# Performance work log

Hardware: AMD Instinct MI355X
Metric: run time of the kernel (lower is better)

Reference implementation:

```python
import jax, jax.numpy as jnp
import numpy as np

H_IMG, W_IMG = 224, 224  # image_size default in forward


def setup_inputs() -> dict:
    key = jax.random.key(0)
    k0, k1, k2 = jax.random.split(key, 3)
    B, C, M, N = 4, 256, 1024, 16384
    xyz_feats = jax.random.normal(k0, (B, C, M), jnp.float32)
    # projections land inside the image for a realistic bin distribution
    points = jax.random.uniform(k1, (B, N, 3), jnp.float32).at[..., 2].add(0.5)
    centers = jax.random.uniform(k2, (B, M, 3), jnp.float32).at[..., 2].add(0.5)
    fx = fy = 0.5 * W_IMG  # plausible intrinsics already scaled to 224x224
    K = jnp.array([[fx, 0.0, W_IMG / 2.0],
                   [0.0, fy, H_IMG / 2.0],
                   [0.0, 0.0, 1.0]], jnp.float32)
    return {"xyz_feats": xyz_feats, "points": points, "centers": centers,
            "K": K, "kernel_size": 4}


def reference(xyz_feats, points, centers, K, kernel_size):
    B, C, M = xyz_feats.shape
    N = points.shape[1]
    H, W = H_IMG, W_IMG

    # --- interpolating_points: PointNet++ 3-NN inverse-distance interp ---
    # squared pairwise distances [B, N, M]
    d2 = (jnp.sum(points * points, -1)[:, :, None]
          + jnp.sum(centers * centers, -1)[:, None, :]
          - 2.0 * jnp.einsum('bnd,bmd->bnm', points, centers))
    neg_d, idx = jax.lax.top_k(-d2, 3)            # 3 nearest centers, [B,N,3]
    w = 1.0 / (-neg_d + 1e-8)                     # inverse-distance weights
    w = w / jnp.sum(w, -1, keepdims=True)
    b3 = jnp.arange(B)[:, None, None]
    gathered = xyz_feats[b3, :, idx]              # [B, N, 3, C]
    interp = jnp.einsum('bnkc,bnk->bnc', gathered, w)  # [B, N, C]

    # --- project_to_image ---
    uvz = jnp.einsum('ij,bnj->bni', K, points)    # [B, N, 3]
    uv = uvz[..., :2] / jnp.maximum(uvz[..., 2:], 1e-8)
    u = jnp.clip(jnp.floor(uv[..., 0]), 0, W - 1).astype(jnp.int32)
    v = jnp.clip(jnp.floor(uv[..., 1]), 0, H - 1).astype(jnp.int32)
    idx_flat = u + v * W                          # [B, N]

    # --- scatter-add binning + count normalize ---
    bb = jnp.arange(B)[:, None]
    feat_map = jnp.zeros((B, H * W, C), interp.dtype).at[bb, idx_flat].add(interp)
    count = jnp.zeros((B, H * W), interp.dtype).at[bb, idx_flat].add(1.0)
    feat_map = feat_map / jnp.maximum(count, 1.0)[..., None]
    feat_map = feat_map.reshape(B, H, W, C).transpose(0, 3, 1, 2)  # [B,C,H,W]

    # --- avg_pool2d(kernel_size, stride=kernel_size) ---
    k = kernel_size
    out = feat_map.reshape(B, C, H // k, k, W // k, k).mean(axis=(3, 5))
    return out
```

## Files before the change

### kernel.cpp

```cpp
#include <hip/hip_runtime.h>
#include <hip/hip_bf16.h>

#define H_IMG 224
#define W_IMG 224
#define B_ 4
#define C_ 256
#define M_ 1024
#define N_ 16384
#define HW_ (H_IMG * W_IMG)
#define OH_ 56
#define OW_ 56
#define NBLK_ (OH_ * OW_)
#define NBINS_ (B_ * NBLK_)
#define NT_ (B_ * N_)
#define SEG_ 32
#define MAXSEG_ (NBINS_ + NT_ / SEG_)
#define KS_ 8
#define MC_ (M_ / KS_)
#define PTS_ 128
#define ZTOT_ (NBINS_ * C_ + B_ * HW_ + 2 * NBINS_ + 1)

__global__ __launch_bounds__(1024) void transpose_kernel(
    const float* __restrict__ xyz, float* __restrict__ XT,
    float* __restrict__ zeroRegion)
{
    __shared__ float tile[32][33];
    int b  = blockIdx.z;
    int c0 = blockIdx.x * 32;
    int m0 = blockIdx.y * 32;
    int tx = threadIdx.x, ty = threadIdx.y;
    int flat = ((blockIdx.z * gridDim.y + blockIdx.y) * gridDim.x + blockIdx.x)
               * 1024 + ty * 32 + tx;
    for (int i = flat; i < ZTOT_; i += 1024 * 1024) zeroRegion[i] = 0.0f;
    tile[ty][tx] = xyz[(b * C_ + c0 + ty) * M_ + m0 + tx];
    __syncthreads();
    XT[(b * M_ + m0 + ty) * C_ + c0 + tx] = tile[tx][ty];
}

__global__ __launch_bounds__(1024, 8) void top3_kernel(
    const float* __restrict__ points, const float* __restrict__ centers,
    const float* __restrict__ Kmat,
    int* __restrict__ pixA, int* __restrict__ idA, float* __restrict__ wA,
    float* __restrict__ cnt, int* __restrict__ binCnt)
{
#pragma clang fp contract(off)
    __shared__ float4 cen[M_];
    __shared__ float  pd[KS_][PTS_][3];
    __shared__ int    pi[KS_][PTS_][3];
    int b     = blockIdx.y;
    int t     = threadIdx.x;
    int pl    = t & 127;
    int s     = t >> 7;
    int nbase = blockIdx.x * PTS_;

    {
        const float* cb = centers + (size_t)(b * M_ + t) * 3;
        float cx = cb[0], cy = cb[1], cz = cb[2];
        float c2 = ((cx * cx) + (cy * cy)) + (cz * cz);
        cen[t] = make_float4(cx, cy, cz, c2);
    }
    __syncthreads();

    int g0 = b * N_ + nbase + pl;
    const float* pp = points + (size_t)g0 * 3;
    float px = pp[0], py = pp[1], pz = pp[2];
    float p2 = ((px * px) + (py * py)) + (pz * pz);

    float d0 = 1e30f, d1 = 1e30f, d2v = 1e30f;
    int   i0 = 0, i1 = 0, i2 = 0;
    int mbase = s * MC_;
#pragma unroll 4
    for (int j = 0; j < MC_; ++j) {
        int m = mbase + j;
        float4 cc = cen[m];
        float dot = ((pz * cc.z) + (py * cc.y)) + (px * cc.x);
        float d   = (p2 + cc.w) - (2.0f * dot);
        bool  c0  = d < d0;
        float l0  = fmaxf(d, d0);
        int   li0 = c0 ? i0 : m;
        d0 = fminf(d, d0);
        i0 = c0 ? m : i0;
        bool  c1  = l0 < d1;
        float l1  = fmaxf(l0, d1);
        int   li1 = c1 ? i1 : li0;
        d1 = fminf(l0, d1);
        i1 = c1 ? li0 : i1;
        bool  c2  = l1 < d2v;
        d2v = fminf(l1, d2v);
        i2  = c2 ? li1 : i2;
    }
    pd[s][pl][0] = d0;  pd[s][pl][1] = d1;  pd[s][pl][2] = d2v;
    pi[s][pl][0] = i0;  pi[s][pl][1] = i1;  pi[s][pl][2] = i2;
    __syncthreads();

    if (t < PTS_) {
        float md0 = 1e30f, md1 = 1e30f, md2 = 1e30f;
        int   mi0 = M_,    mi1 = M_,    mi2 = M_;
#pragma unroll
        for (int ss = 0; ss < KS_; ++ss)
#pragma unroll
            for (int j = 0; j < 3; ++j) {
                float dd = pd[ss][t][j];
                int   ii = pi[ss][t][j];
                if ((dd < md2) || (dd == md2 && ii < mi2)) {
                    if ((dd < md1) || (dd == md1 && ii < mi1)) {
                        md2 = md1; mi2 = mi1;
                        if ((dd < md0) || (dd == md0 && ii < mi0)) {
                            md1 = md0; mi1 = mi0; md0 = dd; mi0 = ii;
                        } else { md1 = dd; mi1 = ii; }
                    } else { md2 = dd; mi2 = ii; }
                }
            }

        float w0 = 1.0f / (md0 + 1e-8f);
        float w1 = 1.0f / (md1 + 1e-8f);
        float w2 = 1.0f / (md2 + 1e-8f);
        float ws = (w0 + w1) + w2;
        w0 /= ws; w1 /= ws; w2 /= ws;

        int g = b * N_ + nbase + t;
        const float* pq = points + (size_t)g * 3;
        float qx = pq[0], qy = pq[1], qz = pq[2];
        float fx = Kmat[0], cxk = Kmat[2], fy = Kmat[4], cyk = Kmat[5];
        float u_num = (cxk * qz) + (fx * qx);
        float v_num = (cyk * qz) + (fy * qy);
        float zc    = fmaxf(qz, 1e-8f);
        float u = floorf(u_num / zc);
        float v = floorf(v_num / zc);
        int ui = (int)fminf(fmaxf(u, 0.0f), (float)(W_IMG - 1));
        int vi = (int)fminf(fmaxf(v, 0.0f), (float)(H_IMG - 1));
        int pix = vi * W_IMG + ui;

        pixA[g] = pix;
        idA[g]           = mi0; idA[g + NT_]     = mi1; idA[g + 2 * NT_] = mi2;
        wA [g]           = w0;  wA [g + NT_]     = w1;  wA [g + 2 * NT_] = w2;
        atomicAdd(&cnt[b * HW_ + pix], 1.0f);
        int bin = b * NBLK_ + (vi >> 2) * OW_ + (ui >> 2);
        atomicAdd(&binCnt[bin], 1);
    }
}

__global__ __launch_bounds__(1024) void scan_kernel(
    const int* __restrict__ binCnt, int* __restrict__ binOff,
    int4* __restrict__ segs, int* __restrict__ segTotal)
{
    const int PER = (NBINS_ + 1023) / 1024;
    __shared__ int partK[1024], partS[1024];
    int t = threadIdx.x;
    int base = t * PER;
    int localK[PER], localS[PER];
    int sk = 0, sn = 0;
#pragma unroll
    for (int j = 0; j < PER; ++j) {
        int idx = base + j;
        int k  = (idx < NBINS_) ? binCnt[idx] : 0;
        int ns = 0;
        if (idx < NBINS_) { ns = (k + SEG_ - 1) / SEG_; if (ns == 0) ns = 1; }
        localK[j] = sk; localS[j] = sn;
        sk += k; sn += ns;
    }
    partK[t] = sk; partS[t] = sn;
    __syncthreads();
    for (int ofs = 1; ofs < 1024; ofs <<= 1) {
        int vK = (t >= ofs) ? partK[t - ofs] : 0;
        int vS = (t >= ofs) ? partS[t - ofs] : 0;
        __syncthreads();
        partK[t] += vK; partS[t] += vS;
        __syncthreads();
    }
    int exK = (t == 0) ? 0 : partK[t - 1];
    int exS = (t == 0) ? 0 : partS[t - 1];
#pragma unroll
    for (int j = 0; j < PER; ++j) {
        int idx = base + j;
        if (idx >= NBINS_) continue;
        int off = exK + localK[j];
        int sb  = exS + localS[j];
        binOff[idx] = off;
        int k = binCnt[idx];
        int nseg = (k + SEG_ - 1) / SEG_; if (nseg == 0) nseg = 1;
        for (int q = 0; q < nseg; ++q) {
            int len = k - q * SEG_;
            len = (len < 0) ? 0 : ((len > SEG_) ? SEG_ : len);
            segs[sb + q] = make_int4(idx, off + q * SEG_, len, nseg);
        }
    }
    if (t == 0) segTotal[0] = partS[1023];
}

__global__ __launch_bounds__(256) void pack_kernel(
    const int* __restrict__ pixA, const int* __restrict__ idA,
    const float* __restrict__ wA, const float* __restrict__ cnt,
    const int* __restrict__ binOff, int* __restrict__ binFill,
    int4* __restrict__ idP, float4* __restrict__ wP)
{
    int g = blockIdx.x * 256 + threadIdx.x;
    int b = g >> 14;
    int pix = pixA[g];
    int u = pix % W_IMG, v = pix / W_IMG;
    int bin = b * NBLK_ + (v >> 2) * OW_ + (u >> 2);
    int pos = atomicAdd(&binFill[bin], 1);
    int dst = binOff[bin] + pos;
    float s = 0.0625f / fmaxf(cnt[b * HW_ + pix], 1.0f);
    idP[dst] = make_int4(idA[g], idA[g + NT_], idA[g + 2 * NT_], b);
    wP[dst]  = make_float4(wA[g] * s, wA[g + NT_] * s, wA[g + 2 * NT_] * s, 0.0f);
}

__global__ __launch_bounds__(256) void gather_kernel(
    const float* __restrict__ XT, const int4* __restrict__ segs,
    const int* __restrict__ segTotal, const int4* __restrict__ idP,
    const float4* __restrict__ wP, float* __restrict__ tmp)
{
    int sid = blockIdx.x;
    if (sid >= segTotal[0]) return;
    int4 sg   = segs[sid];
    int bin   = sg.x, start = sg.y, len = sg.z, nseg = sg.w;
    int b     = bin / NBLK_;
    int c     = threadIdx.x;

    __shared__ int4   sId[SEG_];
    __shared__ float4 sW [SEG_];
    if (c < len) { sId[c] = idP[start + c]; sW[c] = wP[start + c]; }
    __syncthreads();

    const float* XTb = XT + (size_t)b * (M_ * C_);
    float accA = 0.0f, accB = 0.0f;
    int j = 0;
    for (; j + 1 < len; j += 2) {
        int4 ia = sId[j];     float4 wa = sW[j];
        int4 ib = sId[j + 1]; float4 wb = sW[j + 1];
        accA = fmaf(wa.x, XTb[ia.x * C_ + c],
               fmaf(wa.y, XTb[ia.y * C_ + c],
               fmaf(wa.z, XTb[ia.z * C_ + c], accA)));
        accB = fmaf(wb.x, XTb[ib.x * C_ + c],
               fmaf(wb.y, XTb[ib.y * C_ + c],
               fmaf(wb.z, XTb[ib.z * C_ + c], accB)));
    }
    if (j < len) {
        int4 ia = sId[j]; float4 wa = sW[j];
        accA = fmaf(wa.x, XTb[ia.x * C_ + c],
               fmaf(wa.y, XTb[ia.y * C_ + c],
               fmaf(wa.z, XTb[ia.z * C_ + c], accA)));
    }
    float acc = accA + accB;

    float* dst = &tmp[(size_t)bin * C_ + c];
    if (nseg == 1) *dst = acc;
    else           atomicAdd(dst, acc);
}

__global__ __launch_bounds__(1024) void untranspose_kernel(
    const float* __restrict__ tmp, float* __restrict__ out)
{
    __shared__ float tile[32][33];
    int b  = blockIdx.z;
    int n0 = blockIdx.x * 32;
    int c0 = blockIdx.y * 32;
    int tx = threadIdx.x, ty = threadIdx.y;
    tile[ty][tx] = tmp[((size_t)b * NBLK_ + n0 + ty) * C_ + c0 + tx];
    __syncthreads();
    out[((size_t)(b * C_ + c0 + ty)) * NBLK_ + n0 + tx] = tile[tx][ty];
}

extern "C" void kernel_launch(void* const* d_in, const int* in_sizes, int n_in,
                              void* d_out, int out_size, void* d_ws, size_t ws_size,
                              hipStream_t stream)
{
    const float* xyz_feats = (const float*)d_in[0];
    const float* points    = (const float*)d_in[1];
    const float* centers   = (const float*)d_in[2];
    const float* Kmat      = (const float*)d_in[3];

    float* out = (float*)d_out;

    float*  XT       = (float*)d_ws;
    int4*   idP      = (int4*)(XT + (size_t)B_ * M_ * C_);
    float4* wP       = (float4*)(idP + NT_);
    int4*   segs     = (int4*)(wP + NT_);
    float*  tmp      = (float*)(segs + MAXSEG_);
    float*  cnt      = tmp + (size_t)NBINS_ * C_;
    int*    binCnt   = (int*)(cnt + (size_t)B_ * HW_);
    int*    binFill  = binCnt + NBINS_;
    int*    segTotal = binFill + NBINS_;
    int*    pixA     = segTotal + 1;
    int*    idA      = pixA + NT_;
    float*  wA       = (float*)(idA + 3 * NT_);
    int*    binOff   = (int*)(wA + 3 * NT_);

    dim3 tb(32, 32);
    dim3 tg(C_ / 32, M_ / 32, B_);
    transpose_kernel<<<tg, tb, 0, stream>>>(xyz_feats, XT, tmp);

    dim3 bg(N_ / PTS_, B_);
    top3_kernel<<<bg, 1024, 0, stream>>>(points, centers, Kmat,
                                         pixA, idA, wA, cnt, binCnt);

    scan_kernel<<<1, 1024, 0, stream>>>(binCnt, binOff, segs, segTotal);

    pack_kernel<<<NT_ / 256, 256, 0, stream>>>(pixA, idA, wA, cnt,
                                               binOff, binFill, idP, wP);

    gather_kernel<<<MAXSEG_, 256, 0, stream>>>(XT, segs, segTotal,
                                               idP, wP, tmp);

    dim3 ug(NBLK_ / 32, C_ / 32, B_);
    untranspose_kernel<<<ug, tb, 0, stream>>>(tmp, out);
}
```

Measured before the change: 186.9 us.

## Fuse scan into top3 via last-block pattern, halve top3 block, widen gather unroll

```diff
diff --git a/kernel.cpp b/kernel.cpp
--- a/kernel.cpp
+++ b/kernel.cpp
@@ -17,8 +17,11 @@
 #define MAXSEG_ (NBINS_ + NT_ / SEG_)
 #define KS_ 8
 #define MC_ (M_ / KS_)
-#define PTS_ 128
-#define ZTOT_ (NBINS_ * C_ + B_ * HW_ + 2 * NBINS_ + 1)
+#define PTS_ 64
+#define TPB3_ (PTS_ * KS_)
+#define NBLK3_ (B_ * N_ / PTS_)
+#define SPER_ ((NBINS_ + TPB3_ - 1) / TPB3_)
+#define ZTOT_ (NBINS_ * C_ + B_ * HW_ + 2 * NBINS_ + 2)
 
 __global__ __launch_bounds__(1024) void transpose_kernel(
     const float* __restrict__ xyz, float* __restrict__ XT,
@@ -37,27 +40,30 @@
     XT[(b * M_ + m0 + ty) * C_ + c0 + tx] = tile[tx][ty];
 }
 
-__global__ __launch_bounds__(1024, 8) void top3_kernel(
+__global__ __launch_bounds__(TPB3_, 8) void top3_kernel(
     const float* __restrict__ points, const float* __restrict__ centers,
     const float* __restrict__ Kmat,
     int* __restrict__ pixA, int* __restrict__ idA, float* __restrict__ wA,
-    float* __restrict__ cnt, int* __restrict__ binCnt)
+    float* __restrict__ cnt, int* __restrict__ binCnt,
+    int* __restrict__ binOff, int4* __restrict__ segs,
+    int* __restrict__ segTotal, int* __restrict__ doneCnt)
 {
 #pragma clang fp contract(off)
     __shared__ float4 cen[M_];
     __shared__ float  pd[KS_][PTS_][3];
     __shared__ int    pi[KS_][PTS_][3];
+    __shared__ int    isLast;
     int b     = blockIdx.y;
     int t     = threadIdx.x;
-    int pl    = t & 127;
-    int s     = t >> 7;
+    int pl    = t & (PTS_ - 1);
+    int s     = t >> 6;
     int nbase = blockIdx.x * PTS_;
 
-    {
-        const float* cb = centers + (size_t)(b * M_ + t) * 3;
+    for (int i = t; i < M_; i += TPB3_) {
+        const float* cb = centers + (size_t)(b * M_ + i) * 3;
         float cx = cb[0], cy = cb[1], cz = cb[2];
         float c2 = ((cx * cx) + (cy * cy)) + (cz * cz);
-        cen[t] = make_float4(cx, cy, cz, c2);
+        cen[i] = make_float4(cx, cy, cz, c2);
     }
     __syncthreads();
 
@@ -138,54 +144,54 @@
         int bin = b * NBLK_ + (vi >> 2) * OW_ + (ui >> 2);
         atomicAdd(&binCnt[bin], 1);
     }
-}
-
-__global__ __launch_bounds__(1024) void scan_kernel(
-    const int* __restrict__ binCnt, int* __restrict__ binOff,
-    int4* __restrict__ segs, int* __restrict__ segTotal)
-{
-    const int PER = (NBINS_ + 1023) / 1024;
-    __shared__ int partK[1024], partS[1024];
-    int t = threadIdx.x;
-    int base = t * PER;
-    int localK[PER], localS[PER];
+
+    __syncthreads();
+    __threadfence();
+    if (t == 0) {
+        int prev = atomicAdd(doneCnt, 1);
+        isLast = (prev == NBLK3_ - 1);
+    }
+    __syncthreads();
+    if (!isLast) return;
+    __threadfence();
+
+    int* partK = &pi[0][0][0];
+    int* partS = partK + TPB3_;
+    int base = t * SPER_;
     int sk = 0, sn = 0;
-#pragma unroll
-    for (int j = 0; j < PER; ++j) {
+    for (int j = 0; j < SPER_; ++j) {
         int idx = base + j;
-        int k  = (idx < NBINS_) ? binCnt[idx] : 0;
-        int ns = 0;
-        if (idx < NBINS_) { ns = (k + SEG_ - 1) / SEG_; if (ns == 0) ns = 1; }
-        localK[j] = sk; localS[j] = sn;
-        sk += k; sn += ns;
+        if (idx < NBINS_) {
+            int k = binCnt[idx];
+            int ns = (k + SEG_ - 1) / SEG_; if (ns == 0) ns = 1;
+            sk += k; sn += ns;
+        }
     }
     partK[t] = sk; partS[t] = sn;
     __syncthreads();
-    for (int ofs = 1; ofs < 1024; ofs <<= 1) {
+    for (int ofs = 1; ofs < TPB3_; ofs <<= 1) {
         int vK = (t >= ofs) ? partK[t - ofs] : 0;
         int vS = (t >= ofs) ? partS[t - ofs] : 0;
         __syncthreads();
         partK[t] += vK; partS[t] += vS;
         __syncthreads();
     }
-    int exK = (t == 0) ? 0 : partK[t - 1];
-    int exS = (t == 0) ? 0 : partS[t - 1];
-#pragma unroll
-    for (int j = 0; j < PER; ++j) {
+    int runK = (t == 0) ? 0 : partK[t - 1];
+    int runS = (t == 0) ? 0 : partS[t - 1];
+    for (int j = 0; j < SPER_; ++j) {
         int idx = base + j;
         if (idx >= NBINS_) continue;
-        int off = exK + localK[j];
-        int sb  = exS + localS[j];
-        binOff[idx] = off;
         int k = binCnt[idx];
-        int nseg = (k + SEG_ - 1) / SEG_; if (nseg == 0) nseg = 1;
-        for (int q = 0; q < nseg; ++q) {
+        int ns = (k + SEG_ - 1) / SEG_; if (ns == 0) ns = 1;
+        binOff[idx] = runK;
+        for (int q = 0; q < ns; ++q) {
             int len = k - q * SEG_;
             len = (len < 0) ? 0 : ((len > SEG_) ? SEG_ : len);
-            segs[sb + q] = make_int4(idx, off + q * SEG_, len, nseg);
+            segs[runS + q] = make_int4(idx, runK + q * SEG_, len, ns);
         }
-    }
-    if (t == 0) segTotal[0] = partS[1023];
+        runK += k; runS += ns;
+    }
+    if (t == TPB3_ - 1) segTotal[0] = partS[TPB3_ - 1];
 }
 
 __global__ __launch_bounds__(256) void pack_kernel(
@@ -224,25 +230,33 @@
     __syncthreads();
 
     const float* XTb = XT + (size_t)b * (M_ * C_);
-    float accA = 0.0f, accB = 0.0f;
+    float a0 = 0.0f, a1 = 0.0f, a2 = 0.0f, a3 = 0.0f;
     int j = 0;
-    for (; j + 1 < len; j += 2) {
-        int4 ia = sId[j];     float4 wa = sW[j];
-        int4 ib = sId[j + 1]; float4 wb = sW[j + 1];
-        accA = fmaf(wa.x, XTb[ia.x * C_ + c],
-               fmaf(wa.y, XTb[ia.y * C_ + c],
-               fmaf(wa.z, XTb[ia.z * C_ + c], accA)));
-        accB = fmaf(wb.x, XTb[ib.x * C_ + c],
-               fmaf(wb.y, XTb[ib.y * C_ + c],
-               fmaf(wb.z, XTb[ib.z * C_ + c], accB)));
-    }
-    if (j < len) {
-        int4 ia = sId[j]; float4 wa = sW[j];
-        accA = fmaf(wa.x, XTb[ia.x * C_ + c],
-               fmaf(wa.y, XTb[ia.y * C_ + c],
-               fmaf(wa.z, XTb[ia.z * C_ + c], accA)));
-    }
-    float acc = accA + accB;
+    for (; j + 3 < len; j += 4) {
+        int4 iA = sId[j];     float4 wAa = sW[j];
+        int4 iB = sId[j + 1]; float4 wBb = sW[j + 1];
+        int4 iC = sId[j + 2]; float4 wCc = sW[j + 2];
+        int4 iD = sId[j + 3]; float4 wDd = sW[j + 3];
+        a0 = fmaf(wAa.x, XTb[iA.x * C_ + c],
+             fmaf(wAa.y, XTb[iA.y * C_ + c],
+             fmaf(wAa.z, XTb[iA.z * C_ + c], a0)));
+        a1 = fmaf(wBb.x, XTb[iB.x * C_ + c],
+             fmaf(wBb.y, XTb[iB.y * C_ + c],
+             fmaf(wBb.z, XTb[iB.z * C_ + c], a1)));
+        a2 = fmaf(wCc.x, XTb[iC.x * C_ + c],
+             fmaf(wCc.y, XTb[iC.y * C_ + c],
+             fmaf(wCc.z, XTb[iC.z * C_ + c], a2)));
+        a3 = fmaf(wDd.x, XTb[iD.x * C_ + c],
+             fmaf(wDd.y, XTb[iD.y * C_ + c],
+             fmaf(wDd.z, XTb[iD.z * C_ + c], a3)));
+    }
+    for (; j < len; ++j) {
+        int4 iA = sId[j]; float4 wAa = sW[j];
+        a0 = fmaf(wAa.x, XTb[iA.x * C_ + c],
+             fmaf(wAa.y, XTb[iA.y * C_ + c],
+             fmaf(wAa.z, XTb[iA.z * C_ + c], a0)));
+    }
+    float acc = (a0 + a1) + (a2 + a3);
 
     float* dst = &tmp[(size_t)bin * C_ + c];
     if (nseg == 1) *dst = acc;
@@ -282,7 +296,8 @@
     int*    binCnt   = (int*)(cnt + (size_t)B_ * HW_);
     int*    binFill  = binCnt + NBINS_;
     int*    segTotal = binFill + NBINS_;
-    int*    pixA     = segTotal + 1;
+    int*    doneCnt  = segTotal + 1;
+    int*    pixA     = doneCnt + 1;
     int*    idA      = pixA + NT_;
     float*  wA       = (float*)(idA + 3 * NT_);
     int*    binOff   = (int*)(wA + 3 * NT_);
@@ -292,10 +307,9 @@
     transpose_kernel<<<tg, tb, 0, stream>>>(xyz_feats, XT, tmp);
 
     dim3 bg(N_ / PTS_, B_);
-    top3_kernel<<<bg, 1024, 0, stream>>>(points, centers, Kmat,
-                                         pixA, idA, wA, cnt, binCnt);
-
-    scan_kernel<<<1, 1024, 0, stream>>>(binCnt, binOff, segs, segTotal);
+    top3_kernel<<<bg, TPB3_, 0, stream>>>(points, centers, Kmat,
+                                          pixA, idA, wA, cnt, binCnt,
+                                          binOff, segs, segTotal, doneCnt);
 
     pack_kernel<<<NT_ / 256, 256, 0, stream>>>(pixA, idA, wA, cnt,
                                                binOff, binFill, idP, wP);
```

Result: slower. 285.4 us (+52.7%).
